# Kernel optimization log

Measured on AMD Instinct MI355X. Metric: run time of the kernel, lower is better.

Reference implementation:

```python
import jax, jax.numpy as jnp
import numpy as np

B, N, D, H = 8, 2048, 256, 4
HD = D // H


def setup_inputs() -> dict:
    key = jax.random.key(0)
    ks = jax.random.split(key, 12)
    s = 1.0 / np.sqrt(D)
    inp = {
        "node_features": jax.random.normal(ks[0], (B, N, D), dtype=jnp.float32),
        "causal_mask": jnp.tril(jnp.ones((N, N), dtype=jnp.float32)),
        "Wq": jax.random.normal(ks[1], (D, D), dtype=jnp.float32) * s,
        "bq": jnp.zeros((D,), dtype=jnp.float32),
        "Wk": jax.random.normal(ks[2], (D, D), dtype=jnp.float32) * s,
        "bk": jnp.zeros((D,), dtype=jnp.float32),
        "Wv": jax.random.normal(ks[3], (D, D), dtype=jnp.float32) * s,
        "bv": jnp.zeros((D,), dtype=jnp.float32),
        "Wo": jax.random.normal(ks[4], (D, D), dtype=jnp.float32) * s,
        "bo": jnp.zeros((D,), dtype=jnp.float32),
        "Wu": jax.random.normal(ks[5], (2 * D, D), dtype=jnp.float32) * (1.0 / np.sqrt(2 * D)),
        "bu": jnp.zeros((D,), dtype=jnp.float32),
    }
    return inp


def reference(node_features, causal_mask, Wq, bq, Wk, bk, Wv, bv, Wo, bo, Wu, bu):
    # node_features: [B, N, D]; causal_mask: [N, N] (1 = keep, 0 = masked)
    x = node_features
    # project and split heads -> [B, H, N, HD]
    def heads(w, b):
        return (x @ w + b).reshape(B, N, H, HD).transpose(0, 2, 1, 3)
    q, k, v = heads(Wq, bq), heads(Wk, bk), heads(Wv, bv)
    scale = 1.0 / np.sqrt(HD).astype(np.float32)
    scores = jnp.einsum("bhnd,bhmd->bhnm", q, k) * scale  # [B, H, N, N]
    scores = jnp.where(causal_mask > 0, scores, jnp.float32(-1e9))
    attn = jax.nn.softmax(scores, axis=-1)
    ctx = jnp.einsum("bhnm,bhmd->bhnd", attn, v)  # [B, H, N, HD]
    messages = ctx.transpose(0, 2, 1, 3).reshape(B, N, D) @ Wo + bo  # [B, N, D]
    combined = jnp.concatenate([x, messages], axis=-1)  # [B, N, 2D]
    updated = jax.nn.relu(combined @ Wu + bu)  # [B, N, D]  (dropout = identity in eval)
    return updated
```

## Files before the change

### kernel.cpp

```cpp
#include <hip/hip_runtime.h>
#include <math.h>

constexpr int B  = 8;
constexpr int N  = 2048;
constexpr int D  = 256;
constexpr int H  = 4;
constexpr int HD = 64;
constexpr int MTOT = B * N;

typedef __attribute__((ext_vector_type(8))) short  short8;
typedef __attribute__((ext_vector_type(4))) float  floatx4;
typedef unsigned short ushort_t;

#define QSCALE 0.1803368801111204f

__device__ __forceinline__ unsigned short f2bf(float f) {
    unsigned u = __float_as_uint(f);
    u += 0x7fffu + ((u >> 16) & 1u);
    return (unsigned short)(u >> 16);
}

__device__ __forceinline__ unsigned short f2bf_t(float f) {
    return (unsigned short)(__float_as_uint(f) >> 16);
}

__device__ __forceinline__ void gl_lds16(const ushort_t* g, ushort_t* l) {
    __builtin_amdgcn_global_load_lds(
        (const __attribute__((address_space(1))) void*)g,
        (__attribute__((address_space(3))) void*)l, 16, 0, 0);
}

__global__ __launch_bounds__(256) void prep(
    const float* __restrict__ x,
    const float* __restrict__ Wq, const float* __restrict__ Wk,
    const float* __restrict__ Wv, const float* __restrict__ Wo,
    const float* __restrict__ Wu,
    ushort_t* __restrict__ xb,
    ushort_t* __restrict__ wqkvt, ushort_t* __restrict__ wut,
    ushort_t* __restrict__ wbt,   ushort_t* __restrict__ wob)
{
    __shared__ float Ls[64][65];
    const int bx = blockIdx.x;
    const int t  = threadIdx.x;

    if (bx < 2048) {
        int idx = (bx * 256 + t) * 8;
        float4 a = *(const float4*)(x + idx);
        float4 b = *(const float4*)(x + idx + 4);
        ushort_t o[8] = {f2bf(a.x), f2bf(a.y), f2bf(a.z), f2bf(a.w),
                         f2bf(b.x), f2bf(b.y), f2bf(b.z), f2bf(b.w)};
        *(short8*)(xb + idx) = *(const short8*)o;
        return;
    }

    if (bx < 2112) {
        const int e  = bx - 2048;
        const int zz = e >> 4;
        const int kt = (e >> 2) & 3;
        const int nt = e & 3;
        const float* src; ushort_t* dst; int K;
        if      (zz == 0) { src = Wq; dst = wqkvt;          K = 256; }
        else if (zz == 1) { src = Wk; dst = wqkvt + 65536;  K = 256; }
        else if (zz == 2) { src = Wv; dst = wqkvt + 131072; K = 256; }
        else              { src = Wu; dst = wut;            K = 512; }
        #pragma unroll
        for (int i = 0; i < 16; i++) {
            int ee = t + i * 256, r = ee >> 6, c = ee & 63;
            Ls[r][c] = src[(size_t)(kt * 64 + r) * 256 + nt * 64 + c];
        }
        __syncthreads();
        #pragma unroll
        for (int i = 0; i < 16; i++) {
            int ee = t + i * 256, r = ee >> 6, c = ee & 63;
            dst[(size_t)(nt * 64 + r) * K + kt * 64 + c] = f2bf(Ls[c][r]);
        }
        return;
    }

    if (bx < 2128) {
        const int e  = bx - 2112;
        const int kt = e >> 2;
        const int nt = e & 3;
        #pragma unroll
        for (int i = 0; i < 16; i++) {
            int ee = t + i * 256, r = ee >> 6, c = ee & 63;
            Ls[r][c] = Wu[(size_t)(256 + kt * 64 + r) * 256 + nt * 64 + c];
        }
        __syncthreads();
        #pragma unroll
        for (int i = 0; i < 16; i++) {
            int ee = t + i * 256, r = ee >> 6, c = ee & 63;
            wbt[(size_t)(nt * 64 + r) * 256 + kt * 64 + c] = f2bf(Ls[c][r]);
        }
        return;
    }

    {
        int idx = ((bx - 2128) * 256 + t) * 8;
        float4 a = *(const float4*)(Wo + idx);
        float4 b = *(const float4*)(Wo + idx + 4);
        ushort_t o[8] = {f2bf(a.x), f2bf(a.y), f2bf(a.z), f2bf(a.w),
                         f2bf(b.x), f2bf(b.y), f2bf(b.z), f2bf(b.w)};
        *(short8*)(wob + idx) = *(const short8*)o;
    }
}

__global__ __launch_bounds__(256) void qkv_gemm(
    const ushort_t* __restrict__ xb, const ushort_t* __restrict__ wqkvt,
    const ushort_t* __restrict__ wob, const ushort_t* __restrict__ wbt,
    const float* __restrict__ Wu,
    const float* __restrict__ bq, const float* __restrict__ bk,
    const float* __restrict__ bv, const float* __restrict__ bo,
    const float* __restrict__ bu,
    ushort_t* __restrict__ q, ushort_t* __restrict__ kout,
    ushort_t* __restrict__ vt,
    ushort_t* __restrict__ wut, float* __restrict__ b2)
{
    __shared__ ushort_t SH[128 * 132];

    const int t = threadIdx.x, w = t >> 6, lane = t & 63;
    const int quad = lane >> 4, l16 = lane & 15;
    const int bx = blockIdx.x;
    const int wr = (w >> 1) * 64, wc = (w & 1) * 64;

    if (blockIdx.y == 128) {
        if (bx < 4) {
            const int row0 = (bx >> 1) * 128;
            const int col0 = (bx & 1) * 128;
            floatx4 acc[4][4] = {};
            const ushort_t* Arow = wob + (size_t)(row0 + wr + l16) * 256 + quad * 8;
            const ushort_t* Brow = wbt + (size_t)(col0 + wc + l16) * 256 + quad * 8;
            #pragma unroll
            for (int k0 = 0; k0 < 256; k0 += 32) {
                short8 af[4], bf[4];
                #pragma unroll
                for (int i = 0; i < 4; i++)
                    af[i] = *(const short8*)(Arow + (size_t)i * 16 * 256 + k0);
                #pragma unroll
                for (int j = 0; j < 4; j++)
                    bf[j] = *(const short8*)(Brow + (size_t)j * 16 * 256 + k0);
                __builtin_amdgcn_s_setprio(1);
                #pragma unroll
                for (int i = 0; i < 4; i++)
                    #pragma unroll
                    for (int j = 0; j < 4; j++)
                        acc[i][j] = __builtin_amdgcn_mfma_f32_16x16x32_bf16(
                            af[i], bf[j], acc[i][j], 0, 0, 0);
                __builtin_amdgcn_s_setprio(0);
            }
            #pragma unroll
            for (int j = 0; j < 4; j++) {
                int cl = wc + j * 16 + l16;
                #pragma unroll
                for (int i = 0; i < 4; i++)
                    #pragma unroll
                    for (int r = 0; r < 4; r++) {
                        int ml = wr + i * 16 + quad * 4 + r;
                        wut[(size_t)(col0 + cl) * 512 + 256 + row0 + ml] =
                            f2bf(acc[i][j][r]);
                    }
            }
        } else if (bx == 4) {
            float s0 = 0.f, s1 = 0.f, s2 = 0.f, s3 = 0.f;
            for (int j = 0; j < 64; j++) {
                s0 = fmaf(bo[j],       Wu[(size_t)(256 + j)       * 256 + t], s0);
                s1 = fmaf(bo[j + 64],  Wu[(size_t)(256 + j + 64)  * 256 + t], s1);
                s2 = fmaf(bo[j + 128], Wu[(size_t)(256 + j + 128) * 256 + t], s2);
                s3 = fmaf(bo[j + 192], Wu[(size_t)(256 + j + 192) * 256 + t], s3);
            }
            b2[t] = bu[t] + ((s0 + s1) + (s2 + s3));
        }
        return;
    }

    const int col0 = bx * 128, row0 = blockIdx.y * 128;

    floatx4 acc[4][4] = {};

    const ushort_t* Arow = xb    + (size_t)(row0 + wr + l16) * 256 + quad * 8;
    const ushort_t* Brow = wqkvt + (size_t)(col0 + wc + l16) * 256 + quad * 8;
    #pragma unroll
    for (int k0 = 0; k0 < 256; k0 += 32) {
        short8 af[4], bf[4];
        #pragma unroll
        for (int i = 0; i < 4; i++)
            af[i] = *(const short8*)(Arow + (size_t)i * 16 * 256 + k0);
        #pragma unroll
        for (int j = 0; j < 4; j++)
            bf[j] = *(const short8*)(Brow + (size_t)j * 16 * 256 + k0);
        __builtin_amdgcn_s_setprio(1);
        #pragma unroll
        for (int i = 0; i < 4; i++)
            #pragma unroll
            for (int j = 0; j < 4; j++)
                acc[i][j] = __builtin_amdgcn_mfma_f32_16x16x32_bf16(
                    af[i], bf[j], acc[i][j], 0, 0, 0);
        __builtin_amdgcn_s_setprio(0);
    }

    const int kind = bx >> 1;
    const float* bias = (kind == 0) ? bq : (kind == 1 ? bk : bv);
    const float scl  = (kind == 0) ? QSCALE : 1.0f;
    ushort_t (*Ts)[132] = (ushort_t(*)[132])SH;
    #pragma unroll
    for (int j = 0; j < 4; j++) {
        int cl = wc + j * 16 + l16;
        float bsv = bias[(bx & 1) * 128 + cl];
        #pragma unroll
        for (int i = 0; i < 4; i++) {
            #pragma unroll
            for (int r = 0; r < 4; r++) {
                int ml = wr + i * 16 + quad * 4 + r;
                ushort_t bvv = f2bf((acc[i][j][r] + bsv) * scl);
                if (kind < 2) Ts[ml][cl] = bvv;
                else          Ts[cl][ml] = bvv;
            }
        }
    }
    __syncthreads();

    const int b = row0 >> 11, n0 = row0 & (N - 1);
    #pragma unroll
    for (int i = 0; i < 8; i++) {
        int id = t + (i << 8);
        int rr = id >> 4, c8 = (id & 15) << 3;
        short8 val = *(const short8*)&Ts[rr][c8];
        if (kind < 2) {
            int cg = (bx & 1) * 128 + c8;
            int h = cg >> 6, hd = cg & 63;
            if (kind == 0) {
                *(short8*)&q[(((size_t)(b * H + h)) * N + n0 + rr) * HD + hd] = val;
            } else {
                int hd2 = (((hd >> 3) ^ (rr & 7)) << 3);
                *(short8*)&kout[(((size_t)(b * H + h)) * N + n0 + rr) * HD + hd2] = val;
            }
        } else {
            int cg = (bx & 1) * 128 + rr;
            int h = cg >> 6, hd = cg & 63;
            int u  = id & 15;
            int up = (u & 8) | ((u ^ hd) & 7);
            *(short8*)&vt[(((size_t)(b * H + h)) * HD + hd) * N + n0 + (up << 3)] = val;
        }
    }
}

__global__ __launch_bounds__(512) void attn_mfma(
    const ushort_t* __restrict__ q,
    const ushort_t* __restrict__ k,
    const ushort_t* __restrict__ vt,
    ushort_t* __restrict__ ctxb)
{
    __shared__ ushort_t Ks [2][128 * 64];
    __shared__ ushort_t Vts[2][64 * 128];
    __shared__ ushort_t Ps [8][16][36];

    const int t    = threadIdx.x;
    const int w    = t >> 6;
    const int lane = t & 63;
    const int quad = lane >> 4;
    const int l16  = lane & 15;
    const int swz  = l16 & 7;
    const int bh   = blockIdx.x;
    const int b    = bh >> 2, h = bh & 3;
    const int by   = blockIdx.y;
    const int grp  = w >> 2;
    const int qt   = grp ? by : (31 - by);
    const int qbase = qt * 64;
    const int rowb  = qbase + (w & 3) * 16;

    const ushort_t* qp = q  + (size_t)bh * N * HD;
    const ushort_t* kp = k  + (size_t)bh * N * HD;
    const ushort_t* vp = vt + (size_t)bh * HD * N;

    short8 qf0, qf1;
    {
        const ushort_t* qrow = qp + (size_t)(rowb + l16) * HD + quad * 8;
        qf0 = *(const short8*)(qrow);
        qf1 = *(const short8*)(qrow + 32);
    }

    floatx4 acc_o[4] = {};
    float plsum[4] = {};

    const int nkt_self = (qt >> 1) + 1;
    const int nkt_max  = ((31 - by) >> 1) + 1;

    #pragma unroll
    for (int i = 0; i < 2; i++) {
        int e = t + (i << 9);
        gl_lds16(kp + (((size_t)(e >> 3)) << 6) + ((e & 7) << 3),
                 &Ks[0][e * 8]);
        gl_lds16(vp + (size_t)(e >> 4) * N + ((e & 15) << 3),
                 &Vts[0][e * 8]);
    }
    __syncthreads();

    for (int kt = 0; kt < nkt_max; kt++) {
        const int kbase = kt * 128;
        const int cur   = kt & 1;

        if (kt + 1 < nkt_max) {
            const int kb2 = kbase + 128;
            #pragma unroll
            for (int i = 0; i < 2; i++) {
                int e = t + (i << 9);
                gl_lds16(kp + (((size_t)(kb2 + (e >> 3))) << 6) + ((e & 7) << 3),
                         &Ks[cur ^ 1][e * 8]);
                gl_lds16(vp + (size_t)(e >> 4) * N + kb2 + ((e & 15) << 3),
                         &Vts[cur ^ 1][e * 8]);
            }
        }

        if (kt < nkt_self) {
            const ushort_t* Ksc  = Ks[cur];
            const ushort_t* Vtsc = Vts[cur];

            int rem = rowb + 15 - kbase;
            int nch = (rem < 0) ? 0 : ((rem >> 5) + 1);
            if (nch > 4) nch = 4;

            for (int ch = 0; ch < nch; ch++) {
                #pragma unroll
                for (int c2 = 0; c2 < 2; c2++) {
                    const int ct = ch * 2 + c2;
                    const int krow = (ct * 16 + l16) * 64;
                    short8 kf0 = *(const short8*)&Ksc[krow + ((quad ^ swz) << 3)];
                    short8 kf1 = *(const short8*)&Ksc[krow + (((4 + quad) ^ swz) << 3)];
                    floatx4 z = {0.0f, 0.0f, 0.0f, 0.0f};
                    __builtin_amdgcn_s_setprio(1);
                    floatx4 s = __builtin_amdgcn_mfma_f32_16x16x32_bf16(qf0, kf0, z, 0, 0, 0);
                    s         = __builtin_amdgcn_mfma_f32_16x16x32_bf16(qf1, kf1, s, 0, 0, 0);
                    __builtin_amdgcn_s_setprio(0);
                    const bool partial = (kbase + ct * 16 + 15) > rowb;
                    if (partial) {
                        const int keyg = kbase + ct * 16 + l16;
                        #pragma unroll
                        for (int r = 0; r < 4; r++) {
                            float sv = s[r];
                            if (keyg > rowb + quad * 4 + r) sv = -3.0e38f;
                            float pv = __builtin_amdgcn_exp2f(sv);
                            plsum[r] += pv;
                            Ps[w][quad * 4 + r][c2 * 16 + l16] = f2bf_t(pv);
                        }
                    } else {
                        #pragma unroll
                        for (int r = 0; r < 4; r++) {
                            float pv = __builtin_amdgcn_exp2f(s[r]);
                            plsum[r] += pv;
                            Ps[w][quad * 4 + r][c2 * 16 + l16] = f2bf_t(pv);
                        }
                    }
                }
                short8 pf = *(const short8*)&Ps[w][l16][quad * 8];
                const int uu = ch * 4 + quad;
                const int up = (uu & 8) | ((uu ^ l16) & 7);
                __builtin_amdgcn_s_setprio(1);
                #pragma unroll
                for (int nt = 0; nt < 4; nt++) {
                    short8 vf = *(const short8*)&Vtsc[(nt * 16 + l16) * 128 + (up << 3)];
                    acc_o[nt] = __builtin_amdgcn_mfma_f32_16x16x32_bf16(pf, vf, acc_o[nt], 0, 0, 0);
                }
                __builtin_amdgcn_s_setprio(0);
            }
        }

        __syncthreads();
    }

    #pragma unroll
    for (int r = 0; r < 4; r++) {
        float l = plsum[r];
        l += __shfl_xor(l, 1);
        l += __shfl_xor(l, 2);
        l += __shfl_xor(l, 4);
        l += __shfl_xor(l, 8);
        float inv = 1.0f / l;
        int   n   = rowb + quad * 4 + r;
        #pragma unroll
        for (int nt = 0; nt < 4; nt++) {
            ctxb[((size_t)(b * N + n)) * D + h * HD + nt * 16 + l16] =
                f2bf(acc_o[nt][r] * inv);
        }
    }
}

__global__ __launch_bounds__(256) void tail2(
    const ushort_t* __restrict__ xb, const ushort_t* __restrict__ ctxb,
    const ushort_t* __restrict__ wut, const float* __restrict__ b2,
    float* __restrict__ out)
{
    __shared__ ushort_t As[2][64 * 64];
    __shared__ ushort_t Bs[2][128 * 64];

    const int t = threadIdx.x, w = t >> 6, lane = t & 63;
    const int quad = lane >> 4, l16 = lane & 15;
    const int col0 = blockIdx.x * 128, row0 = blockIdx.y * 64;
    const int wr = (w >> 1) * 32, wc = (w & 1) * 64;

    floatx4 acc[2][4] = {};

    #pragma unroll
    for (int i = 0; i < 2; i++) {
        int e = t + (i << 8);
        int r = e >> 3, c8 = (e & 7) << 3;
        gl_lds16(xb + (size_t)(row0 + r) * 256 + c8, &As[0][e * 8]);
    }
    #pragma unroll
    for (int i = 0; i < 4; i++) {
        int e = t + (i << 8);
        int r = e >> 3, c8 = (e & 7) << 3;
        gl_lds16(wut + (size_t)(col0 + r) * 512 + c8, &Bs[0][e * 8]);
    }
    __syncthreads();

    for (int ks = 0; ks < 8; ks++) {
        const int cur = ks & 1;
        if (ks < 7) {
            const int k0n = (ks + 1) * 64;
            const ushort_t* Ab = (k0n < 256) ? xb : ctxb;
            const int ka = k0n & 255;
            #pragma unroll
            for (int i = 0; i < 2; i++) {
                int e = t + (i << 8);
                int r = e >> 3, c8 = (e & 7) << 3;
                gl_lds16(Ab + (size_t)(row0 + r) * 256 + ka + c8,
                         &As[cur ^ 1][e * 8]);
            }
            #pragma unroll
            for (int i = 0; i < 4; i++) {
                int e = t + (i << 8);
                int r = e >> 3, c8 = (e & 7) << 3;
                gl_lds16(wut + (size_t)(col0 + r) * 512 + k0n + c8,
                         &Bs[cur ^ 1][e * 8]);
            }
        }

        #pragma unroll
        for (int kk = 0; kk < 64; kk += 32) {
            short8 af[2], bf[4];
            #pragma unroll
            for (int i = 0; i < 2; i++)
                af[i] = *(const short8*)&As[cur][(wr + i * 16 + l16) * 64 + kk + quad * 8];
            #pragma unroll
            for (int j = 0; j < 4; j++)
                bf[j] = *(const short8*)&Bs[cur][(wc + j * 16 + l16) * 64 + kk + quad * 8];
            __builtin_amdgcn_s_setprio(1);
            #pragma unroll
            for (int i = 0; i < 2; i++)
                #pragma unroll
                for (int j = 0; j < 4; j++)
                    acc[i][j] = __builtin_amdgcn_mfma_f32_16x16x32_bf16(
                        af[i], bf[j], acc[i][j], 0, 0, 0);
            __builtin_amdgcn_s_setprio(0);
        }
        __syncthreads();
    }

    #pragma unroll
    for (int j = 0; j < 4; j++) {
        int col = col0 + wc + j * 16 + l16;
        float bsv = b2[col];
        #pragma unroll
        for (int i = 0; i < 2; i++) {
            #pragma unroll
            for (int r = 0; r < 4; r++) {
                int m = row0 + wr + i * 16 + quad * 4 + r;
                out[(size_t)m * 256 + col] = fmaxf(acc[i][j][r] + bsv, 0.0f);
            }
        }
    }
}

extern "C" void kernel_launch(void* const* d_in, const int* in_sizes, int n_in,
                              void* d_out, int out_size, void* d_ws, size_t ws_size,
                              hipStream_t stream)
{
    const float* x  = (const float*)d_in[0];
    const float* Wq = (const float*)d_in[2];
    const float* bq = (const float*)d_in[3];
    const float* Wk = (const float*)d_in[4];
    const float* bk = (const float*)d_in[5];
    const float* Wv = (const float*)d_in[6];
    const float* bv = (const float*)d_in[7];
    const float* Wo = (const float*)d_in[8];
    const float* bo = (const float*)d_in[9];
    const float* Wu = (const float*)d_in[10];
    const float* bu = (const float*)d_in[11];
    float* out = (float*)d_out;

    const size_t SZ = (size_t)MTOT * D;
    ushort_t* xb    = (ushort_t*)d_ws;
    ushort_t* qb    = xb    + SZ;
    ushort_t* kb    = qb    + SZ;
    ushort_t* vbt   = kb    + SZ;
    ushort_t* ctxb  = vbt   + SZ;
    ushort_t* wqkvt = ctxb  + SZ;
    ushort_t* wut   = wqkvt + 196608;
    ushort_t* wbt   = wut   + 131072;
    ushort_t* wob   = wbt   + 65536;
    float*    b2    = (float*)(wob + 65536);

    prep<<<2160, 256, 0, stream>>>(x, Wq, Wk, Wv, Wo, Wu,
                                   xb, wqkvt, wut, wbt, wob);

    qkv_gemm<<<dim3(6, 129), 256, 0, stream>>>(
        xb, wqkvt, wob, wbt, Wu, bq, bk, bv, bo, bu,
        qb, kb, vbt, wut, b2);

    attn_mfma<<<dim3(32, 16), 512, 0, stream>>>(qb, kb, vbt, ctxb);

    tail2<<<dim3(2, 256), 256, 0, stream>>>(xb, ctxb, wut, b2, out);
}
```

Baseline: 181.6 us.

## Split attention blocks to one query tile each and drop K/V double buffering

The attention kernel no longer pairs a long and a short causal query tile in one 512-thread block. It now launches 1024 blocks of 256 threads, one 64-row query tile each. K/V staging becomes single-buffered: each key tile is loaded synchronously between two barriers, replacing the prefetch of the next tile. Shared memory use is halved, which may allow more resident blocks, but global loads no longer overlap compute and per-block work is unbalanced again (scheduled largest-first).

```diff
diff --git a/kernel.cpp b/kernel.cpp
--- a/kernel.cpp
+++ b/kernel.cpp
@@ -244,15 +244,15 @@
     }
 }
 
-__global__ __launch_bounds__(512) void attn_mfma(
+__global__ __launch_bounds__(256) void attn_mfma(
     const ushort_t* __restrict__ q,
     const ushort_t* __restrict__ k,
     const ushort_t* __restrict__ vt,
     ushort_t* __restrict__ ctxb)
 {
-    __shared__ ushort_t Ks [2][128 * 64];
-    __shared__ ushort_t Vts[2][64 * 128];
-    __shared__ ushort_t Ps [8][16][36];
+    __shared__ ushort_t Ks [128 * 64];
+    __shared__ ushort_t Vts[64 * 128];
+    __shared__ ushort_t Ps [4][16][36];
 
     const int t    = threadIdx.x;
     const int w    = t >> 6;
@@ -262,11 +262,9 @@
     const int swz  = l16 & 7;
     const int bh   = blockIdx.x;
     const int b    = bh >> 2, h = bh & 3;
-    const int by   = blockIdx.y;
-    const int grp  = w >> 2;
-    const int qt   = grp ? by : (31 - by);
+    const int qt   = 31 - blockIdx.y;
     const int qbase = qt * 64;
-    const int rowb  = qbase + (w & 3) * 16;
+    const int rowb  = qbase + w * 16;
 
     const ushort_t* qp = q  + (size_t)bh * N * HD;
     const ushort_t* kp = k  + (size_t)bh * N * HD;
@@ -282,89 +280,69 @@
     floatx4 acc_o[4] = {};
     float plsum[4] = {};
 
-    const int nkt_self = (qt >> 1) + 1;
-    const int nkt_max  = ((31 - by) >> 1) + 1;
-
-    #pragma unroll
-    for (int i = 0; i < 2; i++) {
-        int e = t + (i << 9);
-        gl_lds16(kp + (((size_t)(e >> 3)) << 6) + ((e & 7) << 3),
-                 &Ks[0][e * 8]);
-        gl_lds16(vp + (size_t)(e >> 4) * N + ((e & 15) << 3),
-                 &Vts[0][e * 8]);
-    }
-    __syncthreads();
-
-    for (int kt = 0; kt < nkt_max; kt++) {
+    const int nkt = (qt >> 1) + 1;
+
+    for (int kt = 0; kt < nkt; kt++) {
         const int kbase = kt * 128;
-        const int cur   = kt & 1;
-
-        if (kt + 1 < nkt_max) {
-            const int kb2 = kbase + 128;
-            #pragma unroll
-            for (int i = 0; i < 2; i++) {
-                int e = t + (i << 9);
-                gl_lds16(kp + (((size_t)(kb2 + (e >> 3))) << 6) + ((e & 7) << 3),
-                         &Ks[cur ^ 1][e * 8]);
-                gl_lds16(vp + (size_t)(e >> 4) * N + kb2 + ((e & 15) << 3),
-                         &Vts[cur ^ 1][e * 8]);
-            }
-        }
-
-        if (kt < nkt_self) {
-            const ushort_t* Ksc  = Ks[cur];
-            const ushort_t* Vtsc = Vts[cur];
-
-            int rem = rowb + 15 - kbase;
-            int nch = (rem < 0) ? 0 : ((rem >> 5) + 1);
-            if (nch > 4) nch = 4;
-
-            for (int ch = 0; ch < nch; ch++) {
-                #pragma unroll
-                for (int c2 = 0; c2 < 2; c2++) {
-                    const int ct = ch * 2 + c2;
-                    const int krow = (ct * 16 + l16) * 64;
-                    short8 kf0 = *(const short8*)&Ksc[krow + ((quad ^ swz) << 3)];
-                    short8 kf1 = *(const short8*)&Ksc[krow + (((4 + quad) ^ swz) << 3)];
-                    floatx4 z = {0.0f, 0.0f, 0.0f, 0.0f};
-                    __builtin_amdgcn_s_setprio(1);
-                    floatx4 s = __builtin_amdgcn_mfma_f32_16x16x32_bf16(qf0, kf0, z, 0, 0, 0);
-                    s         = __builtin_amdgcn_mfma_f32_16x16x32_bf16(qf1, kf1, s, 0, 0, 0);
-                    __builtin_amdgcn_s_setprio(0);
-                    const bool partial = (kbase + ct * 16 + 15) > rowb;
-                    if (partial) {
-                        const int keyg = kbase + ct * 16 + l16;
-                        #pragma unroll
-                        for (int r = 0; r < 4; r++) {
-                            float sv = s[r];
-                            if (keyg > rowb + quad * 4 + r) sv = -3.0e38f;
-                            float pv = __builtin_amdgcn_exp2f(sv);
-                            plsum[r] += pv;
-                            Ps[w][quad * 4 + r][c2 * 16 + l16] = f2bf_t(pv);
-                        }
-                    } else {
-                        #pragma unroll
-                        for (int r = 0; r < 4; r++) {
-                            float pv = __builtin_amdgcn_exp2f(s[r]);
-                            plsum[r] += pv;
-                            Ps[w][quad * 4 + r][c2 * 16 + l16] = f2bf_t(pv);
-                        }
+        __syncthreads();
+
+        #pragma unroll
+        for (int i = 0; i < 4; i++) {
+            int e = t + (i << 8);
+            gl_lds16(kp + (((size_t)(kbase + (e >> 3))) << 6) + ((e & 7) << 3),
+                     &Ks[e * 8]);
+            gl_lds16(vp + (size_t)(e >> 4) * N + kbase + ((e & 15) << 3),
+                     &Vts[e * 8]);
+        }
+        __syncthreads();
+
+        int rem = rowb + 15 - kbase;
+        int nch = (rem < 0) ? 0 : ((rem >> 5) + 1);
+        if (nch > 4) nch = 4;
+
+        for (int ch = 0; ch < nch; ch++) {
+            #pragma unroll
+            for (int c2 = 0; c2 < 2; c2++) {
+                const int ct = ch * 2 + c2;
+                const int krow = (ct * 16 + l16) * 64;
+                short8 kf0 = *(const short8*)&Ks[krow + ((quad ^ swz) << 3)];
+                short8 kf1 = *(const short8*)&Ks[krow + (((4 + quad) ^ swz) << 3)];
+                floatx4 z = {0.0f, 0.0f, 0.0f, 0.0f};
+                __builtin_amdgcn_s_setprio(1);
+                floatx4 s = __builtin_amdgcn_mfma_f32_16x16x32_bf16(qf0, kf0, z, 0, 0, 0);
+                s         = __builtin_amdgcn_mfma_f32_16x16x32_bf16(qf1, kf1, s, 0, 0, 0);
+                __builtin_amdgcn_s_setprio(0);
+                const bool partial = (kbase + ct * 16 + 15) > rowb;
+                if (partial) {
+                    const int keyg = kbase + ct * 16 + l16;
+                    #pragma unroll
+                    for (int r = 0; r < 4; r++) {
+                        float sv = s[r];
+                        if (keyg > rowb + quad * 4 + r) sv = -3.0e38f;
+                        float pv = __builtin_amdgcn_exp2f(sv);
+                        plsum[r] += pv;
+                        Ps[w][quad * 4 + r][c2 * 16 + l16] = f2bf_t(pv);
+                    }
+                } else {
+                    #pragma unroll
+                    for (int r = 0; r < 4; r++) {
+                        float pv = __builtin_amdgcn_exp2f(s[r]);
+                        plsum[r] += pv;
+                        Ps[w][quad * 4 + r][c2 * 16 + l16] = f2bf_t(pv);
                     }
                 }
-                short8 pf = *(const short8*)&Ps[w][l16][quad * 8];
-                const int uu = ch * 4 + quad;
-                const int up = (uu & 8) | ((uu ^ l16) & 7);
-                __builtin_amdgcn_s_setprio(1);
-                #pragma unroll
-                for (int nt = 0; nt < 4; nt++) {
-                    short8 vf = *(const short8*)&Vtsc[(nt * 16 + l16) * 128 + (up << 3)];
-                    acc_o[nt] = __builtin_amdgcn_mfma_f32_16x16x32_bf16(pf, vf, acc_o[nt], 0, 0, 0);
-                }
-                __builtin_amdgcn_s_setprio(0);
-            }
-        }
-
-        __syncthreads();
+            }
+            short8 pf = *(const short8*)&Ps[w][l16][quad * 8];
+            const int uu = ch * 4 + quad;
+            const int up = (uu & 8) | ((uu ^ l16) & 7);
+            __builtin_amdgcn_s_setprio(1);
+            #pragma unroll
+            for (int nt = 0; nt < 4; nt++) {
+                short8 vf = *(const short8*)&Vts[(nt * 16 + l16) * 128 + (up << 3)];
+                acc_o[nt] = __builtin_amdgcn_mfma_f32_16x16x32_bf16(pf, vf, acc_o[nt], 0, 0, 0);
+            }
+            __builtin_amdgcn_s_setprio(0);
+        }
     }
 
     #pragma unroll
@@ -507,7 +485,7 @@
         xb, wqkvt, wob, wbt, Wu, bq, bk, bv, bo, bu,
         qb, kb, vbt, wut, b2);
 
-    attn_mfma<<<dim3(32, 16), 512, 0, stream>>>(qb, kb, vbt, ctxb);
+    attn_mfma<<<dim3(32, 32), 256, 0, stream>>>(qb, kb, vbt, ctxb);
 
     tail2<<<dim3(2, 256), 256, 0, stream>>>(xb, ctxb, wut, b2, out);
 }
```

New measurement: 186.6 us. 1.03x slower.

## Split causal attention key range across wave halves with LDS reduction

Applied to the files above, without the earlier changes.

Before, each block paired two query tiles (a light one and a heavy one) to balance causal work, with key tiles double-buffered. Now each block handles a single query tile, and the two groups of four waves each process half of the key tiles. Their partial outputs and row sums are combined through shared memory at the end. The grid doubles to 1024 blocks for more parallelism. In exchange, the prefetch double-buffering is lost, since both buffers are loaded synchronously each step, and the final reduction adds extra syncs and LDS traffic.

```diff
diff --git a/kernel.cpp b/kernel.cpp
--- a/kernel.cpp
+++ b/kernel.cpp
@@ -262,11 +262,11 @@
     const int swz  = l16 & 7;
     const int bh   = blockIdx.x;
     const int b    = bh >> 2, h = bh & 3;
-    const int by   = blockIdx.y;
-    const int grp  = w >> 2;
-    const int qt   = grp ? by : (31 - by);
+    const int qt   = 31 - blockIdx.y;
     const int qbase = qt * 64;
-    const int rowb  = qbase + (w & 3) * 16;
+    const int strip = w & 3;
+    const int half  = w >> 2;
+    const int rowb  = qbase + strip * 16;
 
     const ushort_t* qp = q  + (size_t)bh * N * HD;
     const ushort_t* kp = k  + (size_t)bh * N * HD;
@@ -282,104 +282,122 @@
     floatx4 acc_o[4] = {};
     float plsum[4] = {};
 
-    const int nkt_self = (qt >> 1) + 1;
-    const int nkt_max  = ((31 - by) >> 1) + 1;
-
-    #pragma unroll
-    for (int i = 0; i < 2; i++) {
-        int e = t + (i << 9);
-        gl_lds16(kp + (((size_t)(e >> 3)) << 6) + ((e & 7) << 3),
-                 &Ks[0][e * 8]);
-        gl_lds16(vp + (size_t)(e >> 4) * N + ((e & 15) << 3),
-                 &Vts[0][e * 8]);
-    }
-    __syncthreads();
-
-    for (int kt = 0; kt < nkt_max; kt++) {
-        const int kbase = kt * 128;
-        const int cur   = kt & 1;
-
-        if (kt + 1 < nkt_max) {
-            const int kb2 = kbase + 128;
-            #pragma unroll
-            for (int i = 0; i < 2; i++) {
-                int e = t + (i << 9);
-                gl_lds16(kp + (((size_t)(kb2 + (e >> 3))) << 6) + ((e & 7) << 3),
-                         &Ks[cur ^ 1][e * 8]);
-                gl_lds16(vp + (size_t)(e >> 4) * N + kb2 + ((e & 15) << 3),
-                         &Vts[cur ^ 1][e * 8]);
-            }
-        }
-
-        if (kt < nkt_self) {
-            const ushort_t* Ksc  = Ks[cur];
-            const ushort_t* Vtsc = Vts[cur];
-
-            int rem = rowb + 15 - kbase;
-            int nch = (rem < 0) ? 0 : ((rem >> 5) + 1);
-            if (nch > 4) nch = 4;
-
-            for (int ch = 0; ch < nch; ch++) {
-                #pragma unroll
-                for (int c2 = 0; c2 < 2; c2++) {
-                    const int ct = ch * 2 + c2;
-                    const int krow = (ct * 16 + l16) * 64;
-                    short8 kf0 = *(const short8*)&Ksc[krow + ((quad ^ swz) << 3)];
-                    short8 kf1 = *(const short8*)&Ksc[krow + (((4 + quad) ^ swz) << 3)];
-                    floatx4 z = {0.0f, 0.0f, 0.0f, 0.0f};
-                    __builtin_amdgcn_s_setprio(1);
-                    floatx4 s = __builtin_amdgcn_mfma_f32_16x16x32_bf16(qf0, kf0, z, 0, 0, 0);
-                    s         = __builtin_amdgcn_mfma_f32_16x16x32_bf16(qf1, kf1, s, 0, 0, 0);
-                    __builtin_amdgcn_s_setprio(0);
-                    const bool partial = (kbase + ct * 16 + 15) > rowb;
-                    if (partial) {
-                        const int keyg = kbase + ct * 16 + l16;
-                        #pragma unroll
-                        for (int r = 0; r < 4; r++) {
-                            float sv = s[r];
-                            if (keyg > rowb + quad * 4 + r) sv = -3.0e38f;
-                            float pv = __builtin_amdgcn_exp2f(sv);
-                            plsum[r] += pv;
-                            Ps[w][quad * 4 + r][c2 * 16 + l16] = f2bf_t(pv);
-                        }
-                    } else {
-                        #pragma unroll
-                        for (int r = 0; r < 4; r++) {
-                            float pv = __builtin_amdgcn_exp2f(s[r]);
-                            plsum[r] += pv;
-                            Ps[w][quad * 4 + r][c2 * 16 + l16] = f2bf_t(pv);
-                        }
+    const int nkt = (qt >> 1) + 1;
+    const int hh  = (nkt + 1) >> 1;
+
+    for (int i = 0; i < hh; i++) {
+        __syncthreads();
+
+        int klo = i;
+        int khi = hh + i; if (khi >= nkt) khi = i;
+        #pragma unroll
+        for (int ii = 0; ii < 2; ii++) {
+            int e = t + (ii << 9);
+            gl_lds16(kp + (((size_t)(klo * 128 + (e >> 3))) << 6) + ((e & 7) << 3),
+                     &Ks[0][e * 8]);
+            gl_lds16(kp + (((size_t)(khi * 128 + (e >> 3))) << 6) + ((e & 7) << 3),
+                     &Ks[1][e * 8]);
+            gl_lds16(vp + (size_t)(e >> 4) * N + klo * 128 + ((e & 15) << 3),
+                     &Vts[0][e * 8]);
+            gl_lds16(vp + (size_t)(e >> 4) * N + khi * 128 + ((e & 15) << 3),
+                     &Vts[1][e * 8]);
+        }
+        __syncthreads();
+
+        const int my_kt = half ? (hh + i) : i;
+        if (half && (hh + i) >= nkt) continue;
+
+        const int kbase = my_kt * 128;
+        const ushort_t* Ksc  = Ks[half];
+        const ushort_t* Vtsc = Vts[half];
+
+        int rem = rowb + 15 - kbase;
+        int nch = (rem < 0) ? 0 : ((rem >> 5) + 1);
+        if (nch > 4) nch = 4;
+
+        for (int ch = 0; ch < nch; ch++) {
+            #pragma unroll
+            for (int c2 = 0; c2 < 2; c2++) {
+                const int ct = ch * 2 + c2;
+                const int krow = (ct * 16 + l16) * 64;
+                short8 kf0 = *(const short8*)&Ksc[krow + ((quad ^ swz) << 3)];
+                short8 kf1 = *(const short8*)&Ksc[krow + (((4 + quad) ^ swz) << 3)];
+                floatx4 z = {0.0f, 0.0f, 0.0f, 0.0f};
+                __builtin_amdgcn_s_setprio(1);
+                floatx4 s = __builtin_amdgcn_mfma_f32_16x16x32_bf16(qf0, kf0, z, 0, 0, 0);
+                s         = __builtin_amdgcn_mfma_f32_16x16x32_bf16(qf1, kf1, s, 0, 0, 0);
+                __builtin_amdgcn_s_setprio(0);
+                const bool partial = (kbase + ct * 16 + 15) > rowb;
+                if (partial) {
+                    const int keyg = kbase + ct * 16 + l16;
+                    #pragma unroll
+                    for (int r = 0; r < 4; r++) {
+                        float sv = s[r];
+                        if (keyg > rowb + quad * 4 + r) sv = -3.0e38f;
+                        float pv = __builtin_amdgcn_exp2f(sv);
+                        plsum[r] += pv;
+                        Ps[w][quad * 4 + r][c2 * 16 + l16] = f2bf_t(pv);
+                    }
+                } else {
+                    #pragma unroll
+                    for (int r = 0; r < 4; r++) {
+                        float pv = __builtin_amdgcn_exp2f(s[r]);
+                        plsum[r] += pv;
+                        Ps[w][quad * 4 + r][c2 * 16 + l16] = f2bf_t(pv);
                     }
                 }
-                short8 pf = *(const short8*)&Ps[w][l16][quad * 8];
-                const int uu = ch * 4 + quad;
-                const int up = (uu & 8) | ((uu ^ l16) & 7);
-                __builtin_amdgcn_s_setprio(1);
-                #pragma unroll
-                for (int nt = 0; nt < 4; nt++) {
-                    short8 vf = *(const short8*)&Vtsc[(nt * 16 + l16) * 128 + (up << 3)];
-                    acc_o[nt] = __builtin_amdgcn_mfma_f32_16x16x32_bf16(pf, vf, acc_o[nt], 0, 0, 0);
-                }
-                __builtin_amdgcn_s_setprio(0);
-            }
-        }
-
-        __syncthreads();
-    }
-
-    #pragma unroll
-    for (int r = 0; r < 4; r++) {
-        float l = plsum[r];
-        l += __shfl_xor(l, 1);
-        l += __shfl_xor(l, 2);
-        l += __shfl_xor(l, 4);
-        l += __shfl_xor(l, 8);
-        float inv = 1.0f / l;
-        int   n   = rowb + quad * 4 + r;
-        #pragma unroll
-        for (int nt = 0; nt < 4; nt++) {
-            ctxb[((size_t)(b * N + n)) * D + h * HD + nt * 16 + l16] =
-                f2bf(acc_o[nt][r] * inv);
+            }
+            short8 pf = *(const short8*)&Ps[w][l16][quad * 8];
+            const int uu = ch * 4 + quad;
+            const int up = (uu & 8) | ((uu ^ l16) & 7);
+            __builtin_amdgcn_s_setprio(1);
+            #pragma unroll
+            for (int nt = 0; nt < 4; nt++) {
+                short8 vf = *(const short8*)&Vtsc[(nt * 16 + l16) * 128 + (up << 3)];
+                acc_o[nt] = __builtin_amdgcn_mfma_f32_16x16x32_bf16(pf, vf, acc_o[nt], 0, 0, 0);
+            }
+            __builtin_amdgcn_s_setprio(0);
+        }
+    }
+
+    __syncthreads();
+    float* red = (float*)Ks;
+    const int rbase = (strip * 64 + lane) * 21;
+    if (half) {
+        #pragma unroll
+        for (int nt = 0; nt < 4; nt++)
+            #pragma unroll
+            for (int r = 0; r < 4; r++)
+                red[rbase + nt * 4 + r] = acc_o[nt][r];
+        #pragma unroll
+        for (int r = 0; r < 4; r++)
+            red[rbase + 16 + r] = plsum[r];
+    }
+    __syncthreads();
+    if (!half) {
+        #pragma unroll
+        for (int nt = 0; nt < 4; nt++)
+            #pragma unroll
+            for (int r = 0; r < 4; r++)
+                acc_o[nt][r] += red[rbase + nt * 4 + r];
+        #pragma unroll
+        for (int r = 0; r < 4; r++)
+            plsum[r] += red[rbase + 16 + r];
+
+        #pragma unroll
+        for (int r = 0; r < 4; r++) {
+            float l = plsum[r];
+            l += __shfl_xor(l, 1);
+            l += __shfl_xor(l, 2);
+            l += __shfl_xor(l, 4);
+            l += __shfl_xor(l, 8);
+            float inv = 1.0f / l;
+            int   n   = rowb + quad * 4 + r;
+            #pragma unroll
+            for (int nt = 0; nt < 4; nt++) {
+                ctxb[((size_t)(b * N + n)) * D + h * HD + nt * 16 + l16] =
+                    f2bf(acc_o[nt][r] * inv);
+            }
         }
     }
 }
@@ -507,7 +525,7 @@
         xb, wqkvt, wob, wbt, Wu, bq, bk, bv, bo, bu,
         qb, kb, vbt, wut, b2);
 
-    attn_mfma<<<dim3(32, 16), 512, 0, stream>>>(qb, kb, vbt, ctxb);
+    attn_mfma<<<dim3(32, 32), 512, 0, stream>>>(qb, kb, vbt, ctxb);
 
     tail2<<<dim3(2, 256), 256, 0, stream>>>(xb, ctxb, wut, b2, out);
 }
```

New measurement: 183.1 us. About the same (+0.8%).

## Keep attention probabilities in registers via transposed QK^T and 16x16x16 MFMA

Applied to the files above, without the earlier changes.

Swaps the QK^T MFMA operands so each lane holds four consecutive key scores for one query row. The packed bf16 probabilities can then feed a 16x16x16 bf16 MFMA as the A operand directly, which removes the per-wave LDS staging buffer for P and its store/load round trip. V fragments are loaded as 4-wide pieces up front, and the row-sum reduction becomes a cross-quad shuffle. In exchange it issues twice as many smaller PV MFMAs, and when the builtin is missing it falls back to inline asm with manual s_nop hazard padding.

```diff
diff --git a/kernel.cpp b/kernel.cpp
--- a/kernel.cpp
+++ b/kernel.cpp
@@ -9,10 +9,17 @@
 constexpr int MTOT = B * N;
 
 typedef __attribute__((ext_vector_type(8))) short  short8;
+typedef __attribute__((ext_vector_type(4))) short  short4v;
 typedef __attribute__((ext_vector_type(4))) float  floatx4;
 typedef unsigned short ushort_t;
 
 #define QSCALE 0.1803368801111204f
+
+#if defined(__has_builtin)
+#  if __has_builtin(__builtin_amdgcn_mfma_f32_16x16x16bf16_1k)
+#    define HAVE_MFMA16BF16_BUILTIN 1
+#  endif
+#endif
 
 __device__ __forceinline__ unsigned short f2bf(float f) {
     unsigned u = __float_as_uint(f);
@@ -20,8 +27,12 @@
     return (unsigned short)(u >> 16);
 }
 
-__device__ __forceinline__ unsigned short f2bf_t(float f) {
-    return (unsigned short)(__float_as_uint(f) >> 16);
+__device__ __forceinline__ short4v pack4bf(float p0, float p1, float p2, float p3) {
+    unsigned lo = (__float_as_uint(p0) >> 16) | (__float_as_uint(p1) & 0xffff0000u);
+    unsigned hi = (__float_as_uint(p2) >> 16) | (__float_as_uint(p3) & 0xffff0000u);
+    union { unsigned u[2]; short4v s; } c;
+    c.u[0] = lo; c.u[1] = hi;
+    return c.s;
 }
 
 __device__ __forceinline__ void gl_lds16(const ushort_t* g, ushort_t* l) {
@@ -252,7 +263,6 @@
 {
     __shared__ ushort_t Ks [2][128 * 64];
     __shared__ ushort_t Vts[2][64 * 128];
-    __shared__ ushort_t Ps [8][16][36];
 
     const int t    = threadIdx.x;
     const int w    = t >> 6;
@@ -280,7 +290,8 @@
     }
 
     floatx4 acc_o[4] = {};
-    float plsum[4] = {};
+    float lsum = 0.0f;
+    const int qrow = rowb + l16;
 
     const int nkt_self = (qt >> 1) + 1;
     const int nkt_max  = ((31 - by) >> 1) + 1;
@@ -320,6 +331,16 @@
             if (nch > 4) nch = 4;
 
             for (int ch = 0; ch < nch; ch++) {
+                short4v vfa[2][4];
+                #pragma unroll
+                for (int c2 = 0; c2 < 2; c2++) {
+                    const int uu = ch * 4 + c2 * 2 + (quad >> 1);
+                    const int up = (uu & 8) | ((uu ^ swz) & 7);
+                    const int vo = (up << 3) + (quad & 1) * 4;
+                    #pragma unroll
+                    for (int nt = 0; nt < 4; nt++)
+                        vfa[c2][nt] = *(const short4v*)&Vtsc[(nt * 16 + l16) * 128 + vo];
+                }
                 #pragma unroll
                 for (int c2 = 0; c2 < 2; c2++) {
                     const int ct = ch * 2 + c2;
@@ -328,53 +349,52 @@
                     short8 kf1 = *(const short8*)&Ksc[krow + (((4 + quad) ^ swz) << 3)];
                     floatx4 z = {0.0f, 0.0f, 0.0f, 0.0f};
                     __builtin_amdgcn_s_setprio(1);
-                    floatx4 s = __builtin_amdgcn_mfma_f32_16x16x32_bf16(qf0, kf0, z, 0, 0, 0);
-                    s         = __builtin_amdgcn_mfma_f32_16x16x32_bf16(qf1, kf1, s, 0, 0, 0);
+                    floatx4 s = __builtin_amdgcn_mfma_f32_16x16x32_bf16(kf0, qf0, z, 0, 0, 0);
+                    s         = __builtin_amdgcn_mfma_f32_16x16x32_bf16(kf1, qf1, s, 0, 0, 0);
                     __builtin_amdgcn_s_setprio(0);
+                    const int keyb = kbase + ct * 16 + quad * 4;
                     const bool partial = (kbase + ct * 16 + 15) > rowb;
                     if (partial) {
-                        const int keyg = kbase + ct * 16 + l16;
                         #pragma unroll
-                        for (int r = 0; r < 4; r++) {
-                            float sv = s[r];
-                            if (keyg > rowb + quad * 4 + r) sv = -3.0e38f;
-                            float pv = __builtin_amdgcn_exp2f(sv);
-                            plsum[r] += pv;
-                            Ps[w][quad * 4 + r][c2 * 16 + l16] = f2bf_t(pv);
-                        }
-                    } else {
-                        #pragma unroll
-                        for (int r = 0; r < 4; r++) {
-                            float pv = __builtin_amdgcn_exp2f(s[r]);
-                            plsum[r] += pv;
-                            Ps[w][quad * 4 + r][c2 * 16 + l16] = f2bf_t(pv);
-                        }
+                        for (int r = 0; r < 4; r++)
+                            if (keyb + r > qrow) s[r] = -3.0e38f;
                     }
+                    float p0 = __builtin_amdgcn_exp2f(s[0]);
+                    float p1 = __builtin_amdgcn_exp2f(s[1]);
+                    float p2 = __builtin_amdgcn_exp2f(s[2]);
+                    float p3 = __builtin_amdgcn_exp2f(s[3]);
+                    lsum += (p0 + p1) + (p2 + p3);
+                    short4v pa = pack4bf(p0, p1, p2, p3);
+                    __builtin_amdgcn_s_setprio(1);
+#ifdef HAVE_MFMA16BF16_BUILTIN
+                    #pragma unroll
+                    for (int nt = 0; nt < 4; nt++)
+                        acc_o[nt] = __builtin_amdgcn_mfma_f32_16x16x16bf16_1k(
+                            pa, vfa[c2][nt], acc_o[nt], 0, 0, 0);
+#else
+                    #pragma unroll
+                    for (int nt = 0; nt < 4; nt++)
+                        asm volatile("s_nop 1\n\tv_mfma_f32_16x16x16_bf16 %0, %1, %2, %0"
+                            : "+v"(acc_o[nt]) : "v"(pa), "v"(vfa[c2][nt]));
+#endif
+                    __builtin_amdgcn_s_setprio(0);
                 }
-                short8 pf = *(const short8*)&Ps[w][l16][quad * 8];
-                const int uu = ch * 4 + quad;
-                const int up = (uu & 8) | ((uu ^ l16) & 7);
-                __builtin_amdgcn_s_setprio(1);
-                #pragma unroll
-                for (int nt = 0; nt < 4; nt++) {
-                    short8 vf = *(const short8*)&Vtsc[(nt * 16 + l16) * 128 + (up << 3)];
-                    acc_o[nt] = __builtin_amdgcn_mfma_f32_16x16x32_bf16(pf, vf, acc_o[nt], 0, 0, 0);
-                }
-                __builtin_amdgcn_s_setprio(0);
             }
         }
 
         __syncthreads();
     }
 
+#ifndef HAVE_MFMA16BF16_BUILTIN
+    asm volatile("s_nop 7\n\ts_nop 7");
+#endif
+
+    lsum += __shfl_xor(lsum, 16);
+    lsum += __shfl_xor(lsum, 32);
     #pragma unroll
     for (int r = 0; r < 4; r++) {
-        float l = plsum[r];
-        l += __shfl_xor(l, 1);
-        l += __shfl_xor(l, 2);
-        l += __shfl_xor(l, 4);
-        l += __shfl_xor(l, 8);
-        float inv = 1.0f / l;
+        float lv  = __shfl(lsum, quad * 4 + r);
+        float inv = 1.0f / lv;
         int   n   = rowb + quad * 4 + r;
         #pragma unroll
         for (int nt = 0; nt < 4; nt++) {
```

New measurement: 178.8 us. Within noise of the previous version (-1.5%).
